# Performance work log

Measured on AMD Instinct MI355X. Metric: run time of the kernel, lower is better.

Reference implementation:

```python
import jax, jax.numpy as jnp
import numpy as np
from jax import lax

MAX_DECAY = 0.99
EPS = 1e-05
TOPK = 4


def ema_mask_group(moving_avg, new, mask, decay0, cluster_update_num):
    """Faithful port of ema_tensor_mask_group_inplace, including the quirk that
    the Python-level `decay` variable is carried (and possibly shrunk) across
    cluster iterations. Implemented as a lax.scan over clusters carrying decay.
    moving_avg/new: [C] or [C, D]; mask, cluster_update_num: [C].
    """
    def step(decay, xs):
        ma, nw, m, c = xs
        d = jnp.where((m != 0) & (c <= 10.0), decay * c / 10.0, decay)
        out = jnp.where(m != 0, ma * d + nw * (1.0 - d), ma)
        return d, out
    _, out = lax.scan(step, jnp.asarray(decay0, moving_avg.dtype),
                      (moving_avg, new, mask, cluster_update_num))
    return out


def laplace_smoothing(x, n_categories, eps=EPS):
    return (x + eps) / (x.sum() + n_categories * eps)


def setup_inputs() -> dict:
    key = jax.random.key(0)
    k1, k2 = jax.random.split(key)
    N, C, D = 65536, 512, 256
    return {
        "inputs_flatten": jax.random.normal(k1, (N, D), dtype=jnp.float32),
        "dictionary": jax.random.normal(k2, (C, D), dtype=jnp.float32),
        "cluster_size_sum": jnp.zeros((C,), dtype=jnp.float32),
        "cluster_value": jnp.zeros((C, D), dtype=jnp.float32),
        "cluster_update_num": jnp.ones((C,), dtype=jnp.float32),
    }


def reference(inputs_flatten, dictionary, cluster_size_sum, cluster_value,
              cluster_update_num):
    N, D = inputs_flatten.shape
    C = dictionary.shape[0]
    dic = lax.stop_gradient(dictionary)  # dictionary used via .detach()/.data

    # squared euclidean distances [N, C]
    distances = (jnp.sum(inputs_flatten ** 2, axis=1, keepdims=True)
                 + jnp.sum(dic ** 2, axis=1)
                 - 2.0 * jnp.matmul(inputs_flatten, dic.T))

    # ascending sort -> take topK smallest distances
    _, topk_idx = lax.top_k(-distances, TOPK)          # [N, K]
    topk_emb = dic[topk_idx]                            # [N, K, D]
    group_emb = jnp.sum(topk_emb, axis=1) / TOPK        # [N, D]

    # multi-hot encodings via scatter
    rows = jnp.arange(N)[:, None]
    encodings = jnp.zeros((N, C), dtype=jnp.float32).at[rows, topk_idx].set(1.0)

    # ---- training-mode EMA codebook update (single device: all_gather = identity) ----
    x_sg = lax.stop_gradient(inputs_flatten)
    cluster_size = jnp.sum(encodings, axis=0)           # [C]
    cluster_mask = (cluster_size != 0).astype(jnp.float32)
    cluster_update_num_new = cluster_update_num + cluster_mask

    cluster_size_sum_new = ema_mask_group(cluster_size_sum, cluster_size,
                                          cluster_mask, MAX_DECAY,
                                          cluster_update_num_new)
    input_sum = jnp.matmul(encodings.T, x_sg)           # [C, D]
    cluster_value_new = ema_mask_group(cluster_value, input_sum, cluster_mask,
                                       MAX_DECAY, cluster_update_num_new)

    cs = laplace_smoothing(cluster_size_sum_new, C, EPS) * cluster_size_sum_new.sum()
    embed_normalized = jnp.where(cluster_mask[:, None] == 1.0,
                                 cluster_value_new / cs[:, None],
                                 cluster_value_new)
    dictionary_new = embed_normalized                   # world_size == 1

    # straight-through estimator
    group_emb = lax.stop_gradient(group_emb - inputs_flatten) + inputs_flatten
    return (group_emb, topk_idx, dictionary_new, cluster_size_sum_new,
            cluster_value_new, cluster_update_num_new)
```

## Files before the change

### kernel.cpp

```cpp
#include <hip/hip_runtime.h>

#define N_ROWS 65536
#define C_CLUST 512
#define D_DIM 256

#define WS_DICTT   0
#define WS_DSQ     131072
#define WS_XSQ     131584
#define WS_CS      197120
#define WS_DCY     197632
#define WS_ISUM    198144
#define WS_COUNTS  329216
#define WS_OFFSETS 329728
#define WS_FILL    330752
#define WS_ROWLIST 331264

#define OUT_GEMB 0
#define OUT_TOPK 16777216
#define OUT_DICT 17039360
#define OUT_CSS  17170432
#define OUT_CV   17170944
#define OUT_CNUM 17302016

#define BM 128
#define BN 128
#define BK 16
#define ASTRIDE 132

#define RPB 128

__global__ void zero_k(unsigned* counts, unsigned* fill, float* isum) {
    int t = blockIdx.x * blockDim.x + threadIdx.x;
    if (t < 512) { counts[t] = 0u; fill[t] = 0u; }
    if (t < C_CLUST * D_DIM) isum[t] = 0.f;
}

__global__ void prep_dict(const float* __restrict__ dic, float* __restrict__ ws) {
    int c = blockIdx.x, k = threadIdx.x;
    float v = dic[c * D_DIM + k];
    ws[WS_DICTT + k * C_CLUST + c] = v;
    __shared__ float red[256];
    red[k] = v * v;
    __syncthreads();
    for (int s = 128; s > 0; s >>= 1) {
        if (k < s) red[k] += red[k + s];
        __syncthreads();
    }
    if (k == 0) ws[WS_DSQ + c] = red[0];
}

__global__ void row_sq(const float* __restrict__ x, float* __restrict__ ws) {
    int row = blockIdx.x, k = threadIdx.x;
    float v = x[row * D_DIM + k];
    __shared__ float red[256];
    red[k] = v * v;
    __syncthreads();
    for (int s = 128; s > 0; s >>= 1) {
        if (k < s) red[k] += red[k + s];
        __syncthreads();
    }
    if (k == 0) ws[WS_XSQ + row] = red[0];
}

__device__ __forceinline__ void lexCE(float& av, int& ai, float& bv, int& bi) {
    bool sw = (bv < av) || ((bv == av) && (bi < ai));
    float nv0 = sw ? bv : av; int ni0 = sw ? bi : ai;
    float nv1 = sw ? av : bv; int ni1 = sw ? ai : bi;
    av = nv0; ai = ni0; bv = nv1; bi = ni1;
}

__device__ __forceinline__ void merge4(
    float& a0v, int& a0i, float& a1v, int& a1i,
    float& a2v, int& a2i, float& a3v, int& a3i,
    float b0v, int b0i, float b1v, int b1i,
    float b2v, int b2i, float b3v, int b3i)
{
    bool s0 = (b3v < a0v) || ((b3v == a0v) && (b3i < a0i));
    float m0v = s0 ? b3v : a0v; int m0i = s0 ? b3i : a0i;
    bool s1 = (b2v < a1v) || ((b2v == a1v) && (b2i < a1i));
    float m1v = s1 ? b2v : a1v; int m1i = s1 ? b2i : a1i;
    bool s2 = (b1v < a2v) || ((b1v == a2v) && (b1i < a2i));
    float m2v = s2 ? b1v : a2v; int m2i = s2 ? b1i : a2i;
    bool s3 = (b0v < a3v) || ((b0v == a3v) && (b0i < a3i));
    float m3v = s3 ? b0v : a3v; int m3i = s3 ? b0i : a3i;
    lexCE(m0v, m0i, m2v, m2i);
    lexCE(m1v, m1i, m3v, m3i);
    lexCE(m0v, m0i, m1v, m1i);
    lexCE(m2v, m2i, m3v, m3i);
    a0v = m0v; a0i = m0i; a1v = m1v; a1i = m1i;
    a2v = m2v; a2i = m2i; a3v = m3v; a3i = m3i;
}

__global__ __launch_bounds__(256, 2) void gemm_topk(
    const float* __restrict__ x, const float* __restrict__ ws,
    float* __restrict__ out_topk, unsigned* __restrict__ counts)
{
    __shared__ float As[BK * ASTRIDE];
    __shared__ float Bs[BK * BN];
    __shared__ unsigned hist[512];

    const int tid = threadIdx.x;
    const int tx = tid & 15, ty = tid >> 4;
    const int rowBase = blockIdx.x * BM;
    const float* dictT = ws + WS_DICTT;
    const float* dsq = ws + WS_DSQ;
    const float* xsq = ws + WS_XSQ;

    for (int h = tid; h < 512; h += 256) hist[h] = 0u;

    float rv0 = 3.4e38f, rv1 = 3.4e38f, rv2 = 3.4e38f, rv3 = 3.4e38f;
    int ri0 = 0x7FFFFFFF, ri1 = 0x7FFFFFFF, ri2 = 0x7FFFFFFF, ri3 = 0x7FFFFFFF;

    for (int cc = 0; cc < C_CLUST / BN; ++cc) {
        float acc[8][8];
        #pragma unroll
        for (int i = 0; i < 8; ++i)
            #pragma unroll
            for (int j = 0; j < 8; ++j) acc[i][j] = 0.f;

        for (int kb = 0; kb < D_DIM / BK; ++kb) {
            __syncthreads();
            #pragma unroll
            for (int ii = 0; ii < 2; ++ii) {
                int q = tid + ii * 256;
                int r = q >> 2;
                int kk = (q & 3) << 2;
                const float4 v = *reinterpret_cast<const float4*>(
                    &x[(rowBase + r) * D_DIM + kb * BK + kk]);
                As[(kk + 0) * ASTRIDE + r] = v.x;
                As[(kk + 1) * ASTRIDE + r] = v.y;
                As[(kk + 2) * ASTRIDE + r] = v.z;
                As[(kk + 3) * ASTRIDE + r] = v.w;
            }
            #pragma unroll
            for (int ii = 0; ii < 2; ++ii) {
                int q = tid + ii * 256;
                int k = q >> 5;
                int c4 = (q & 31) << 2;
                *reinterpret_cast<float4*>(&Bs[k * BN + c4]) =
                    *reinterpret_cast<const float4*>(
                        &dictT[(kb * BK + k) * C_CLUST + cc * BN + c4]);
            }
            __syncthreads();
            #pragma unroll
            for (int k = 0; k < BK; ++k) {
                float a[8], b[8];
                float4 t0 = *reinterpret_cast<const float4*>(&As[k * ASTRIDE + ty * 8]);
                float4 t1 = *reinterpret_cast<const float4*>(&As[k * ASTRIDE + ty * 8 + 4]);
                float4 u0 = *reinterpret_cast<const float4*>(&Bs[k * BN + tx * 4]);
                float4 u1 = *reinterpret_cast<const float4*>(&Bs[k * BN + 64 + tx * 4]);
                a[0]=t0.x; a[1]=t0.y; a[2]=t0.z; a[3]=t0.w;
                a[4]=t1.x; a[5]=t1.y; a[6]=t1.z; a[7]=t1.w;
                b[0]=u0.x; b[1]=u0.y; b[2]=u0.z; b[3]=u0.w;
                b[4]=u1.x; b[5]=u1.y; b[6]=u1.z; b[7]=u1.w;
                #pragma unroll
                for (int i = 0; i < 8; ++i)
                    #pragma unroll
                    for (int j = 0; j < 8; ++j)
                        acc[i][j] = fmaf(a[i], b[j], acc[i][j]);
            }
        }

        float ds[8];
        #pragma unroll
        for (int j = 0; j < 8; ++j) {
            int col = (j < 4) ? (tx * 4 + j) : (64 + tx * 4 + (j - 4));
            ds[j] = dsq[cc * BN + col];
        }
        #pragma unroll
        for (int i = 0; i < 8; ++i) {
            float xs = xsq[rowBase + ty * 8 + i];
            float l0v = 3.4e38f, l1v = 3.4e38f, l2v = 3.4e38f, l3v = 3.4e38f;
            int l0i = 0x7FFFFFFF, l1i = 0x7FFFFFFF, l2i = 0x7FFFFFFF, l3i = 0x7FFFFFFF;
            #pragma unroll
            for (int j = 0; j < 8; ++j) {
                int col = (j < 4) ? (tx * 4 + j) : (64 + tx * 4 + (j - 4));
                int idx = cc * BN + col;
                float v = __fsub_rn(__fadd_rn(xs, ds[j]),
                                    __fmul_rn(2.0f, acc[i][j]));
                if (v < l3v) {
                    if (v < l2v) {
                        l3v = l2v; l3i = l2i;
                        if (v < l1v) {
                            l2v = l1v; l2i = l1i;
                            if (v < l0v) { l1v = l0v; l1i = l0i; l0v = v; l0i = idx; }
                            else { l1v = v; l1i = idx; }
                        } else { l2v = v; l2i = idx; }
                    } else { l3v = v; l3i = idx; }
                }
            }
            #pragma unroll
            for (int mask = 1; mask <= 8; mask <<= 1) {
                float b0v = __shfl_xor(l0v, mask); int b0i = __shfl_xor(l0i, mask);
                float b1v = __shfl_xor(l1v, mask); int b1i = __shfl_xor(l1i, mask);
                float b2v = __shfl_xor(l2v, mask); int b2i = __shfl_xor(l2i, mask);
                float b3v = __shfl_xor(l3v, mask); int b3i = __shfl_xor(l3i, mask);
                merge4(l0v, l0i, l1v, l1i, l2v, l2i, l3v, l3i,
                       b0v, b0i, b1v, b1i, b2v, b2i, b3v, b3i);
            }
            if ((tx & 7) == i)
                merge4(rv0, ri0, rv1, ri1, rv2, ri2, rv3, ri3,
                       l0v, l0i, l1v, l1i, l2v, l2i, l3v, l3i);
        }
    }

    if (tx < 8) {
        int r = rowBase + ty * 8 + tx;
        out_topk[r * 4 + 0] = (float)ri0;
        out_topk[r * 4 + 1] = (float)ri1;
        out_topk[r * 4 + 2] = (float)ri2;
        out_topk[r * 4 + 3] = (float)ri3;
        atomicAdd(&hist[ri0], 1u);
        atomicAdd(&hist[ri1], 1u);
        atomicAdd(&hist[ri2], 1u);
        atomicAdd(&hist[ri3], 1u);
    }
    __syncthreads();
    for (int h = tid; h < 512; h += 256) {
        unsigned v = hist[h];
        if (v) atomicAdd(&counts[h], v);
    }
}

__global__ void group_emb_k(const float* __restrict__ x, const float* __restrict__ dic,
                            const float* __restrict__ topk, float* __restrict__ out)
{
    int row = blockIdx.x, d = threadIdx.x;
    int i0 = (int)topk[row * 4 + 0];
    int i1 = (int)topk[row * 4 + 1];
    int i2 = (int)topk[row * 4 + 2];
    int i3 = (int)topk[row * 4 + 3];
    float g = __fadd_rn(__fadd_rn(__fadd_rn(dic[i0 * D_DIM + d],
                                            dic[i1 * D_DIM + d]),
                                  dic[i2 * D_DIM + d]),
                        dic[i3 * D_DIM + d]);
    g = __fmul_rn(g, 0.25f);
    float xv = x[row * D_DIM + d];
    out[row * D_DIM + d] = __fadd_rn(__fsub_rn(g, xv), xv);
}

__global__ void prefix_k(const unsigned* __restrict__ counts, unsigned* __restrict__ offsets) {
    __shared__ unsigned s[512];
    int t = threadIdx.x;
    unsigned my = counts[t];
    s[t] = my;
    __syncthreads();
    for (int off = 1; off < 512; off <<= 1) {
        unsigned v = (t >= off) ? s[t - off] : 0u;
        __syncthreads();
        s[t] += v;
        __syncthreads();
    }
    offsets[t] = s[t] - my;
    if (t == 511) offsets[512] = s[511];
}

__global__ void scatter_k(const float* __restrict__ topk, const unsigned* __restrict__ offsets,
                          unsigned* __restrict__ fill, unsigned* __restrict__ rowlist) {
    int row = blockIdx.x * 256 + threadIdx.x;
    #pragma unroll
    for (int k = 0; k < 4; ++k) {
        int c = (int)topk[row * 4 + k];
        unsigned p = atomicAdd(&fill[c], 1u);
        rowlist[offsets[c] + p] = ((unsigned)c << 16) | (unsigned)row;
    }
}

__global__ __launch_bounds__(256, 8) void cluster_sum2_k(
    const float* __restrict__ x, const unsigned* __restrict__ rowlist,
    float* __restrict__ isum)
{
    const int d = threadIdx.x;
    const int base = blockIdx.x * RPB;
    unsigned e0 = rowlist[base];
    int ccur = (int)(e0 >> 16);
    float acc = 0.f;
    #pragma unroll 4
    for (int j = 0; j < RPB; ++j) {
        unsigned e = rowlist[base + j];
        int c = (int)(e >> 16);
        float v = x[(e & 0xFFFFu) * D_DIM + d];
        if (c != ccur) {
            atomicAdd(&isum[ccur * D_DIM + d], acc);
            acc = 0.f;
            ccur = c;
        }
        acc += v;
    }
    atomicAdd(&isum[ccur * D_DIM + d], acc);
}

__global__ void ema_scalar_k(const float* __restrict__ css_in, const float* __restrict__ cnum_in,
                             const unsigned* __restrict__ counts,
                             float* __restrict__ ws, float* __restrict__ out) {
    __shared__ float sdecay[512];
    __shared__ float sred[512];
    __shared__ float scn[512];
    __shared__ unsigned smask[512];
    int t = threadIdx.x;
    unsigned cnt = counts[t];
    float size = (float)cnt;
    float mask = (cnt != 0u) ? 1.f : 0.f;
    float cnum_new = __fadd_rn(cnum_in[t], mask);
    scn[t] = cnum_new;
    smask[t] = cnt;
    __syncthreads();
    if (t == 0) {
        float d = 0.99f;
        for (int c = 0; c < 512; ++c) {
            if (smask[c] != 0u && scn[c] <= 10.0f)
                d = __fmul_rn(d, scn[c]) / 10.0f;
            sdecay[c] = d;
        }
    }
    __syncthreads();
    float d = sdecay[t];
    float css = css_in[t];
    float css_new = (cnt != 0u)
        ? __fadd_rn(__fmul_rn(css, d), __fmul_rn(size, __fsub_rn(1.f, d)))
        : css;
    out[OUT_CSS + t] = css_new;
    out[OUT_CNUM + t] = cnum_new;
    sred[t] = css_new;
    __syncthreads();
    for (int s = 256; s > 0; s >>= 1) {
        if (t < s) sred[t] += sred[t + s];
        __syncthreads();
    }
    float S = sred[0];
    float cs = __fmul_rn(__fdiv_rn(__fadd_rn(css_new, 1e-5f),
                                   __fadd_rn(S, 0.00512f)), S);
    ws[WS_CS + t] = cs;
    ws[WS_DCY + t] = d;
}

__global__ void final_k(const float* __restrict__ cv_in, const float* __restrict__ ws,
                        const unsigned* __restrict__ counts, float* __restrict__ out) {
    int c = blockIdx.x, d = threadIdx.x;
    float isum = ws[WS_ISUM + c * D_DIM + d];
    float dc = ws[WS_DCY + c];
    float cs = ws[WS_CS + c];
    unsigned cnt = counts[c];
    float cv = cv_in[c * D_DIM + d];
    float cvn = (cnt != 0u)
        ? __fadd_rn(__fmul_rn(cv, dc), __fmul_rn(isum, __fsub_rn(1.f, dc)))
        : cv;
    out[OUT_CV + c * D_DIM + d] = cvn;
    out[OUT_DICT + c * D_DIM + d] = (cnt != 0u) ? __fdiv_rn(cvn, cs) : cvn;
}

extern "C" void kernel_launch(void* const* d_in, const int* in_sizes, int n_in,
                              void* d_out, int out_size, void* d_ws, size_t ws_size,
                              hipStream_t stream) {
    const float* x       = (const float*)d_in[0];
    const float* dic     = (const float*)d_in[1];
    const float* css_in  = (const float*)d_in[2];
    const float* cv_in   = (const float*)d_in[3];
    const float* cnum_in = (const float*)d_in[4];
    float* out = (float*)d_out;
    float* ws  = (float*)d_ws;
    unsigned* counts  = (unsigned*)(ws + WS_COUNTS);
    unsigned* offsets = (unsigned*)(ws + WS_OFFSETS);
    unsigned* fill    = (unsigned*)(ws + WS_FILL);
    unsigned* rowlist = (unsigned*)(ws + WS_ROWLIST);

    zero_k<<<C_CLUST * D_DIM / 256, 256, 0, stream>>>(counts, fill, ws + WS_ISUM);
    prep_dict<<<C_CLUST, 256, 0, stream>>>(dic, ws);
    row_sq<<<N_ROWS, 256, 0, stream>>>(x, ws);

    gemm_topk<<<N_ROWS / BM, 256, 0, stream>>>(x, ws, out + OUT_TOPK, counts);

    group_emb_k<<<N_ROWS, 256, 0, stream>>>(x, dic, out + OUT_TOPK, out + OUT_GEMB);
    prefix_k<<<1, 512, 0, stream>>>(counts, offsets);
    scatter_k<<<N_ROWS / 256, 256, 0, stream>>>(out + OUT_TOPK, offsets, fill, rowlist);
    cluster_sum2_k<<<N_ROWS * 4 / RPB, 256, 0, stream>>>(x, rowlist, ws + WS_ISUM);
    ema_scalar_k<<<1, 512, 0, stream>>>(css_in, cnum_in, counts, ws, out);
    final_k<<<C_CLUST, 256, 0, stream>>>(cv_in, ws, counts, out);
}
```

Measured before the change: 636.8 us.

## Double threads per GEMM block with register prefetch and vectorize group embedding

The distance GEMM/top-k kernel now runs 512 threads per block, each computing a 4x8 micro-tile instead of 8x8. The next K-slice of x and the dictionary is prefetched into registers while the current slice is being multiplied. The intent is to raise occupancy and hide global-load latency, at the cost of more LDS traffic per FMA and more shuffle-merge work per output. The group embedding kernel is also rewritten as a grid-stride loop using float4 loads and stores, which cuts the number of blocks launched and the number of memory instructions issued.

```diff
diff --git a/kernel.cpp b/kernel.cpp
--- a/kernel.cpp
+++ b/kernel.cpp
@@ -91,7 +91,7 @@
     a2v = m2v; a2i = m2i; a3v = m3v; a3i = m3i;
 }
 
-__global__ __launch_bounds__(256, 2) void gemm_topk(
+__global__ __launch_bounds__(512, 4) void gemm_topk(
     const float* __restrict__ x, const float* __restrict__ ws,
     float* __restrict__ out_topk, unsigned* __restrict__ counts)
 {
@@ -106,55 +106,53 @@
     const float* dsq = ws + WS_DSQ;
     const float* xsq = ws + WS_XSQ;
 
-    for (int h = tid; h < 512; h += 256) hist[h] = 0u;
+    const int ar = tid >> 2;
+    const int akk = (tid & 3) << 2;
+    const int bk = tid >> 5;
+    const int bc4 = (tid & 31) << 2;
+
+    if (tid < 512) hist[tid] = 0u;
 
     float rv0 = 3.4e38f, rv1 = 3.4e38f, rv2 = 3.4e38f, rv3 = 3.4e38f;
     int ri0 = 0x7FFFFFFF, ri1 = 0x7FFFFFFF, ri2 = 0x7FFFFFFF, ri3 = 0x7FFFFFFF;
 
     for (int cc = 0; cc < C_CLUST / BN; ++cc) {
-        float acc[8][8];
+        float acc[4][8];
         #pragma unroll
-        for (int i = 0; i < 8; ++i)
+        for (int i = 0; i < 4; ++i)
             #pragma unroll
             for (int j = 0; j < 8; ++j) acc[i][j] = 0.f;
 
+        float4 va = *reinterpret_cast<const float4*>(
+            &x[(rowBase + ar) * D_DIM + akk]);
+        float4 vb = *reinterpret_cast<const float4*>(
+            &dictT[bk * C_CLUST + cc * BN + bc4]);
+
         for (int kb = 0; kb < D_DIM / BK; ++kb) {
             __syncthreads();
-            #pragma unroll
-            for (int ii = 0; ii < 2; ++ii) {
-                int q = tid + ii * 256;
-                int r = q >> 2;
-                int kk = (q & 3) << 2;
-                const float4 v = *reinterpret_cast<const float4*>(
-                    &x[(rowBase + r) * D_DIM + kb * BK + kk]);
-                As[(kk + 0) * ASTRIDE + r] = v.x;
-                As[(kk + 1) * ASTRIDE + r] = v.y;
-                As[(kk + 2) * ASTRIDE + r] = v.z;
-                As[(kk + 3) * ASTRIDE + r] = v.w;
+            As[(akk + 0) * ASTRIDE + ar] = va.x;
+            As[(akk + 1) * ASTRIDE + ar] = va.y;
+            As[(akk + 2) * ASTRIDE + ar] = va.z;
+            As[(akk + 3) * ASTRIDE + ar] = va.w;
+            *reinterpret_cast<float4*>(&Bs[bk * BN + bc4]) = vb;
+            __syncthreads();
+            if (kb + 1 < D_DIM / BK) {
+                va = *reinterpret_cast<const float4*>(
+                    &x[(rowBase + ar) * D_DIM + (kb + 1) * BK + akk]);
+                vb = *reinterpret_cast<const float4*>(
+                    &dictT[((kb + 1) * BK + bk) * C_CLUST + cc * BN + bc4]);
             }
             #pragma unroll
-            for (int ii = 0; ii < 2; ++ii) {
-                int q = tid + ii * 256;
-                int k = q >> 5;
-                int c4 = (q & 31) << 2;
-                *reinterpret_cast<float4*>(&Bs[k * BN + c4]) =
-                    *reinterpret_cast<const float4*>(
-                        &dictT[(kb * BK + k) * C_CLUST + cc * BN + c4]);
-            }
-            __syncthreads();
-            #pragma unroll
             for (int k = 0; k < BK; ++k) {
-                float a[8], b[8];
-                float4 t0 = *reinterpret_cast<const float4*>(&As[k * ASTRIDE + ty * 8]);
-                float4 t1 = *reinterpret_cast<const float4*>(&As[k * ASTRIDE + ty * 8 + 4]);
+                float a[4], b[8];
+                float4 t0 = *reinterpret_cast<const float4*>(&As[k * ASTRIDE + ty * 4]);
                 float4 u0 = *reinterpret_cast<const float4*>(&Bs[k * BN + tx * 4]);
                 float4 u1 = *reinterpret_cast<const float4*>(&Bs[k * BN + 64 + tx * 4]);
                 a[0]=t0.x; a[1]=t0.y; a[2]=t0.z; a[3]=t0.w;
-                a[4]=t1.x; a[5]=t1.y; a[6]=t1.z; a[7]=t1.w;
                 b[0]=u0.x; b[1]=u0.y; b[2]=u0.z; b[3]=u0.w;
                 b[4]=u1.x; b[5]=u1.y; b[6]=u1.z; b[7]=u1.w;
                 #pragma unroll
-                for (int i = 0; i < 8; ++i)
+                for (int i = 0; i < 4; ++i)
                     #pragma unroll
                     for (int j = 0; j < 8; ++j)
                         acc[i][j] = fmaf(a[i], b[j], acc[i][j]);
@@ -168,8 +166,8 @@
             ds[j] = dsq[cc * BN + col];
         }
         #pragma unroll
-        for (int i = 0; i < 8; ++i) {
-            float xs = xsq[rowBase + ty * 8 + i];
+        for (int i = 0; i < 4; ++i) {
+            float xs = xsq[rowBase + ty * 4 + i];
             float l0v = 3.4e38f, l1v = 3.4e38f, l2v = 3.4e38f, l3v = 3.4e38f;
             int l0i = 0x7FFFFFFF, l1i = 0x7FFFFFFF, l2i = 0x7FFFFFFF, l3i = 0x7FFFFFFF;
             #pragma unroll
@@ -198,14 +196,14 @@
                 merge4(l0v, l0i, l1v, l1i, l2v, l2i, l3v, l3i,
                        b0v, b0i, b1v, b1i, b2v, b2i, b3v, b3i);
             }
-            if ((tx & 7) == i)
+            if ((tx & 3) == i)
                 merge4(rv0, ri0, rv1, ri1, rv2, ri2, rv3, ri3,
                        l0v, l0i, l1v, l1i, l2v, l2i, l3v, l3i);
         }
     }
 
-    if (tx < 8) {
-        int r = rowBase + ty * 8 + tx;
+    if (tx < 4) {
+        int r = rowBase + ty * 4 + tx;
         out_topk[r * 4 + 0] = (float)ri0;
         out_topk[r * 4 + 1] = (float)ri1;
         out_topk[r * 4 + 2] = (float)ri2;
@@ -216,27 +214,49 @@
         atomicAdd(&hist[ri3], 1u);
     }
     __syncthreads();
-    for (int h = tid; h < 512; h += 256) {
-        unsigned v = hist[h];
-        if (v) atomicAdd(&counts[h], v);
-    }
-}
-
-__global__ void group_emb_k(const float* __restrict__ x, const float* __restrict__ dic,
-                            const float* __restrict__ topk, float* __restrict__ out)
+    if (tid < 512) {
+        unsigned v = hist[tid];
+        if (v) atomicAdd(&counts[tid], v);
+    }
+}
+
+__global__ __launch_bounds__(256) void group_emb_k(
+    const float* __restrict__ x, const float* __restrict__ dic,
+    const float* __restrict__ topk, float* __restrict__ out)
 {
-    int row = blockIdx.x, d = threadIdx.x;
-    int i0 = (int)topk[row * 4 + 0];
-    int i1 = (int)topk[row * 4 + 1];
-    int i2 = (int)topk[row * 4 + 2];
-    int i3 = (int)topk[row * 4 + 3];
-    float g = __fadd_rn(__fadd_rn(__fadd_rn(dic[i0 * D_DIM + d],
-                                            dic[i1 * D_DIM + d]),
-                                  dic[i2 * D_DIM + d]),
-                        dic[i3 * D_DIM + d]);
-    g = __fmul_rn(g, 0.25f);
-    float xv = x[row * D_DIM + d];
-    out[row * D_DIM + d] = __fadd_rn(__fsub_rn(g, xv), xv);
+    const int stride = gridDim.x * blockDim.x;
+    for (int gid = blockIdx.x * blockDim.x + threadIdx.x;
+         gid < N_ROWS * (D_DIM / 4); gid += stride) {
+        int row = gid >> 6;
+        int d4 = (gid & 63) << 2;
+        int i0 = (int)topk[row * 4 + 0];
+        int i1 = (int)topk[row * 4 + 1];
+        int i2 = (int)topk[row * 4 + 2];
+        int i3 = (int)topk[row * 4 + 3];
+        float4 a = *reinterpret_cast<const float4*>(&dic[i0 * D_DIM + d4]);
+        float4 b = *reinterpret_cast<const float4*>(&dic[i1 * D_DIM + d4]);
+        float4 c = *reinterpret_cast<const float4*>(&dic[i2 * D_DIM + d4]);
+        float4 e = *reinterpret_cast<const float4*>(&dic[i3 * D_DIM + d4]);
+        float4 xv = *reinterpret_cast<const float4*>(&x[row * D_DIM + d4]);
+        float4 o;
+        {
+            float g = __fmul_rn(__fadd_rn(__fadd_rn(__fadd_rn(a.x, b.x), c.x), e.x), 0.25f);
+            o.x = __fadd_rn(__fsub_rn(g, xv.x), xv.x);
+        }
+        {
+            float g = __fmul_rn(__fadd_rn(__fadd_rn(__fadd_rn(a.y, b.y), c.y), e.y), 0.25f);
+            o.y = __fadd_rn(__fsub_rn(g, xv.y), xv.y);
+        }
+        {
+            float g = __fmul_rn(__fadd_rn(__fadd_rn(__fadd_rn(a.z, b.z), c.z), e.z), 0.25f);
+            o.z = __fadd_rn(__fsub_rn(g, xv.z), xv.z);
+        }
+        {
+            float g = __fmul_rn(__fadd_rn(__fadd_rn(__fadd_rn(a.w, b.w), c.w), e.w), 0.25f);
+            o.w = __fadd_rn(__fsub_rn(g, xv.w), xv.w);
+        }
+        *reinterpret_cast<float4*>(&out[row * D_DIM + d4]) = o;
+    }
 }
 
 __global__ void prefix_k(const unsigned* __restrict__ counts, unsigned* __restrict__ offsets) {
@@ -368,9 +388,9 @@
     prep_dict<<<C_CLUST, 256, 0, stream>>>(dic, ws);
     row_sq<<<N_ROWS, 256, 0, stream>>>(x, ws);
 
-    gemm_topk<<<N_ROWS / BM, 256, 0, stream>>>(x, ws, out + OUT_TOPK, counts);
-
-    group_emb_k<<<N_ROWS, 256, 0, stream>>>(x, dic, out + OUT_TOPK, out + OUT_GEMB);
+    gemm_topk<<<N_ROWS / BM, 512, 0, stream>>>(x, ws, out + OUT_TOPK, counts);
+
+    group_emb_k<<<4096, 256, 0, stream>>>(x, dic, out + OUT_TOPK, out + OUT_GEMB);
     prefix_k<<<1, 512, 0, stream>>>(counts, offsets);
     scatter_k<<<N_ROWS / 256, 256, 0, stream>>>(out + OUT_TOPK, offsets, fill, rowlist);
     cluster_sum2_k<<<N_ROWS * 4 / RPB, 256, 0, stream>>>(x, rowlist, ws + WS_ISUM);
```

New measurement: 623.7 us. -2.1%, faster.
